# Kernel optimization log

Measured on AMD Instinct MI355X. Metric: run time of the kernel, lower is better.

## Reference

```python
import jax, jax.numpy as jnp
import numpy as np

DIM = 1024
B, S = 4, 4096

def setup_inputs() -> dict:
    key = jax.random.key(0)
    ks = jax.random.split(key, 8)
    scale = 1.0 / np.sqrt(DIM)
    x = jax.random.normal(ks[0], (B, S, DIM), dtype=jnp.float32)
    Wk = jax.random.normal(ks[1], (DIM, DIM), dtype=jnp.float32) * scale
    Wv = jax.random.normal(ks[2], (DIM, DIM), dtype=jnp.float32) * scale
    Wr = jax.random.normal(ks[3], (DIM, DIM), dtype=jnp.float32) * scale
    Wo = jax.random.normal(ks[4], (DIM, DIM), dtype=jnp.float32) * scale
    time_decay = jax.random.normal(ks[5], (DIM,), dtype=jnp.float32) * 0.01 - 5.0
    time_first = jax.random.normal(ks[6], (DIM,), dtype=jnp.float32) * 0.01
    return {"x": x, "Wk": Wk, "Wv": Wv, "Wr": Wr, "Wo": Wo,
            "time_decay": time_decay, "time_first": time_first}

def reference(x, Wk, Wv, Wr, Wo, time_decay, time_first):
    # Projections (Linear with weight [out, in]: y = x @ W^T)
    k = jnp.einsum('bsd,ed->bse', x, Wk)
    v = jnp.einsum('bsd,ed->bse', x, Wv)
    r = jax.nn.sigmoid(jnp.einsum('bsd,ed->bse', x, Wr))
    w = -jnp.exp(time_decay)          # (D,)
    decay = jnp.exp(w)                # exp(w), per-channel decay in (0,1)
    eu = jnp.exp(time_first)          # exp(u)
    kv = k * v                        # (B, S, D)

    def step(state, kv_t):
        wkv = state + eu * kv_t       # output numerator this step
        new_state = decay * state + kv_t
        return new_state, wkv

    state0 = jnp.zeros((x.shape[0], x.shape[2]), dtype=x.dtype)
    # scan over time axis: move S to leading dim
    _, wkv_seq = jax.lax.scan(step, state0, jnp.swapaxes(kv, 0, 1))  # (S, B, D)
    out = r * jnp.swapaxes(wkv_seq, 0, 1)  # (B, S, D)
    return jnp.einsum('bsd,ed->bse', out, Wo)
```

## Files before the change

### kernel.cpp

```cpp
#include <hip/hip_runtime.h>
#include <hip/hip_bf16.h>

#define DIMD   1024
#define BATCH  4
#define SEQ    4096
#define NTOK   (BATCH * SEQ)
#define CHUNK  64
#define NCHUNK (SEQ / CHUNK)

#define BM 128
#define BN 128
#define BK 32
#define BNF 64

typedef unsigned short ushort_t;
typedef __attribute__((ext_vector_type(8))) __bf16   bf16x8;
typedef __attribute__((ext_vector_type(4))) float    f32x4;
typedef __attribute__((ext_vector_type(8))) ushort_t u16x8;

__device__ __forceinline__ float b2f(ushort_t u) {
    union { unsigned int i; float f; } x;
    x.i = ((unsigned int)u) << 16;
    return x.f;
}

__device__ __forceinline__ ushort_t f2b(float f) {
    union { float f; unsigned int i; } x;
    x.f = f;
    unsigned int r = x.i + 0x7fffu + ((x.i >> 16) & 1u);
    return (ushort_t)(r >> 16);
}

__global__ __launch_bounds__(256)
void conv_f2b(const float* __restrict__ src, ushort_t* __restrict__ dst, int n8)
{
    const int i = blockIdx.x * 256 + threadIdx.x;
    if (i >= n8) return;
    const float4* s4 = (const float4*)src;
    const float4 a = s4[i * 2];
    const float4 b = s4[i * 2 + 1];
    u16x8 o;
    o[0] = f2b(a.x); o[1] = f2b(a.y); o[2] = f2b(a.z); o[3] = f2b(a.w);
    o[4] = f2b(b.x); o[5] = f2b(b.y); o[6] = f2b(b.z); o[7] = f2b(b.w);
    *(u16x8*)(dst + (size_t)i * 8) = o;
}

__global__ __launch_bounds__(256)
void conv_w(const float* __restrict__ W0, const float* __restrict__ W1,
            const float* __restrict__ W2, const float* __restrict__ W3,
            ushort_t* __restrict__ dst)
{
    const int m = blockIdx.y;
    const float* src = (m == 0) ? W0 : (m == 1) ? W1 : (m == 2) ? W2 : W3;
    const int i = blockIdx.x * 256 + threadIdx.x;
    const float4* s4 = (const float4*)src;
    const float4 a = s4[i * 2];
    const float4 b = s4[i * 2 + 1];
    u16x8 o;
    o[0] = f2b(a.x); o[1] = f2b(a.y); o[2] = f2b(a.z); o[3] = f2b(a.w);
    o[4] = f2b(b.x); o[5] = f2b(b.y); o[6] = f2b(b.z); o[7] = f2b(b.w);
    *(u16x8*)(dst + (size_t)m * DIMD * DIMD + (size_t)i * 8) = o;
}

__global__ __launch_bounds__(256, 2)
void gemm_kvr(const ushort_t* __restrict__ A,
              const ushort_t* __restrict__ Wk,
              const ushort_t* __restrict__ Wv,
              const ushort_t* __restrict__ Wr,
              const float* __restrict__ td,
              ushort_t* __restrict__ Okv,
              ushort_t* __restrict__ Or,
              float* __restrict__ cs)
{
    __shared__ __align__(16) ushort_t As[BM * BK];
    __shared__ __align__(16) ushort_t Bk[BNF * BK];
    __shared__ __align__(16) ushort_t Bv[BNF * BK];
    __shared__ __align__(16) ushort_t Br[BNF * BK];

    const int tid  = threadIdx.x;
    const int lane = tid & 63;
    const int wv   = tid >> 6;
    const int wr   = wv >> 1;
    const int wc   = wv & 1;
    const int lrow = lane & 15;
    const int kq   = lane >> 4;

    const int row0 = blockIdx.x * BM;
    const int e0   = blockIdx.y * BNF;

    f32x4 ak[4][2], av[4][2], ar[4][2];
#pragma unroll
    for (int i = 0; i < 4; i++)
#pragma unroll
        for (int j = 0; j < 2; j++) {
            ak[i][j] = f32x4{0.f, 0.f, 0.f, 0.f};
            av[i][j] = f32x4{0.f, 0.f, 0.f, 0.f};
            ar[i][j] = f32x4{0.f, 0.f, 0.f, 0.f};
        }

    for (int kt = 0; kt < DIMD / BK; ++kt) {
        const int k0 = kt * BK;

        __syncthreads();

#pragma unroll
        for (int it = 0; it < 2; ++it) {
            const int chunk = tid + it * 256;
            const int r = chunk >> 2;
            const int c = (chunk & 3) << 3;
            const ushort_t* ga = A + (size_t)(row0 + r) * DIMD + k0 + c;
            __builtin_amdgcn_global_load_lds(
                (__attribute__((address_space(1))) void*)ga,
                (__attribute__((address_space(3))) void*)((char*)As + chunk * 16),
                16, 0, 0);
        }
        {
            const int r = tid >> 2;
            const int c = (tid & 3) << 3;
            const size_t go = (size_t)(e0 + r) * DIMD + k0 + c;
            __builtin_amdgcn_global_load_lds(
                (__attribute__((address_space(1))) void*)(Wk + go),
                (__attribute__((address_space(3))) void*)((char*)Bk + tid * 16),
                16, 0, 0);
            __builtin_amdgcn_global_load_lds(
                (__attribute__((address_space(1))) void*)(Wv + go),
                (__attribute__((address_space(3))) void*)((char*)Bv + tid * 16),
                16, 0, 0);
            __builtin_amdgcn_global_load_lds(
                (__attribute__((address_space(1))) void*)(Wr + go),
                (__attribute__((address_space(3))) void*)((char*)Br + tid * 16),
                16, 0, 0);
        }

        __syncthreads();

        bf16x8 af[4], bk4[2], bv4[2], br4[2];
#pragma unroll
        for (int i = 0; i < 4; i++)
            af[i] = *(const bf16x8*)(As + (wr * 64 + i * 16 + lrow) * BK + kq * 8);
#pragma unroll
        for (int j = 0; j < 2; j++) {
            const int bo = (wc * 32 + j * 16 + lrow) * BK + kq * 8;
            bk4[j] = *(const bf16x8*)(Bk + bo);
            bv4[j] = *(const bf16x8*)(Bv + bo);
            br4[j] = *(const bf16x8*)(Br + bo);
        }

#pragma unroll
        for (int i = 0; i < 4; i++)
#pragma unroll
            for (int j = 0; j < 2; j++) {
                ak[i][j] = __builtin_amdgcn_mfma_f32_16x16x32_bf16(
                    af[i], bk4[j], ak[i][j], 0, 0, 0);
                av[i][j] = __builtin_amdgcn_mfma_f32_16x16x32_bf16(
                    af[i], bv4[j], av[i][j], 0, 0, 0);
                ar[i][j] = __builtin_amdgcn_mfma_f32_16x16x32_bf16(
                    af[i], br4[j], ar[i][j], 0, 0, 0);
            }
    }

#pragma unroll
    for (int i = 0; i < 4; i++)
#pragma unroll
        for (int j = 0; j < 2; j++)
#pragma unroll
            for (int r = 0; r < 4; r++) {
                const int row = row0 + wr * 64 + i * 16 + kq * 4 + r;
                const int col = e0 + wc * 32 + j * 16 + lrow;
                const size_t o = (size_t)row * DIMD + col;
                Okv[o] = f2b(ak[i][j][r] * av[i][j][r]);
                Or[o]  = f2b(1.f / (1.f + __expf(-ar[i][j][r])));
            }

#pragma unroll
    for (int j = 0; j < 2; j++) {
        const int col = e0 + wc * 32 + j * 16 + lrow;
        const float w = -__expf(td[col]);
        float s = 0.f;
#pragma unroll
        for (int i = 0; i < 4; i++)
#pragma unroll
            for (int r = 0; r < 4; r++) {
                const int rl = i * 16 + kq * 4 + r;
                s += __expf(w * (float)(63 - rl)) * ak[i][j][r] * av[i][j][r];
            }
        s += __shfl_xor(s, 16);
        s += __shfl_xor(s, 32);
        if (kq == 0) {
            const int gchunk = (row0 >> 6) + wr;
            cs[(size_t)gchunk * DIMD + col] = s;
        }
    }
}

__global__ __launch_bounds__(256, 2)
void gemm_bt(const ushort_t* __restrict__ A,
             const ushort_t* __restrict__ W,
             float* __restrict__ Of)
{
    __shared__ __align__(16) ushort_t As[BM * BK];
    __shared__ __align__(16) ushort_t Bs[BN * BK];

    const int tid  = threadIdx.x;
    const int lane = tid & 63;
    const int wv   = tid >> 6;
    const int wr   = wv >> 1;
    const int wc   = wv & 1;
    const int lrow = lane & 15;
    const int kq   = lane >> 4;

    const int row0 = blockIdx.x * BM;
    const int e0   = blockIdx.y * BN;

    f32x4 acc[4][4];
#pragma unroll
    for (int i = 0; i < 4; i++)
#pragma unroll
        for (int j = 0; j < 4; j++)
            acc[i][j] = f32x4{0.f, 0.f, 0.f, 0.f};

    for (int kt = 0; kt < DIMD / BK; ++kt) {
        const int k0 = kt * BK;

        __syncthreads();

#pragma unroll
        for (int it = 0; it < 2; ++it) {
            const int chunk = tid + it * 256;
            const int r = chunk >> 2;
            const int c = (chunk & 3) << 3;
            const ushort_t* ga = A + (size_t)(row0 + r) * DIMD + k0 + c;
            const ushort_t* gb = W + (size_t)(e0 + r) * DIMD + k0 + c;
            __builtin_amdgcn_global_load_lds(
                (__attribute__((address_space(1))) void*)ga,
                (__attribute__((address_space(3))) void*)((char*)As + chunk * 16),
                16, 0, 0);
            __builtin_amdgcn_global_load_lds(
                (__attribute__((address_space(1))) void*)gb,
                (__attribute__((address_space(3))) void*)((char*)Bs + chunk * 16),
                16, 0, 0);
        }

        __syncthreads();

        bf16x8 af[4], bfr[4];
#pragma unroll
        for (int i = 0; i < 4; i++)
            af[i] = *(const bf16x8*)(As + (wr * 64 + i * 16 + lrow) * BK + kq * 8);
#pragma unroll
        for (int j = 0; j < 4; j++)
            bfr[j] = *(const bf16x8*)(Bs + (wc * 64 + j * 16 + lrow) * BK + kq * 8);

#pragma unroll
        for (int i = 0; i < 4; i++)
#pragma unroll
            for (int j = 0; j < 4; j++)
                acc[i][j] = __builtin_amdgcn_mfma_f32_16x16x32_bf16(
                    af[i], bfr[j], acc[i][j], 0, 0, 0);
    }

#pragma unroll
    for (int i = 0; i < 4; i++)
#pragma unroll
        for (int j = 0; j < 4; j++)
#pragma unroll
            for (int r = 0; r < 4; r++) {
                const int row = row0 + wr * 64 + i * 16 + kq * 4 + r;
                const int col = e0 + wc * 64 + j * 16 + lrow;
                Of[(size_t)row * DIMD + col] = acc[i][j][r];
            }
}

__global__ __launch_bounds__(256)
void chunk_scan(float* __restrict__ cs, const float* __restrict__ td)
{
    const int idx = blockIdx.x * 256 + threadIdx.x;
    const int d = idx & (DIMD - 1);
    const int b = idx >> 10;

    const float w      = -__expf(td[d]);
    const float decayL = __expf(w * (float)CHUNK);

    float v[NCHUNK];
    const size_t base = ((size_t)b * NCHUNK) * DIMD + d;
#pragma unroll
    for (int c = 0; c < NCHUNK; c++)
        v[c] = cs[base + (size_t)c * DIMD];

    float st = 0.f;
#pragma unroll
    for (int c = 0; c < NCHUNK; c++) {
        const float sc = v[c];
        v[c] = st;
        st = decayL * st + sc;
    }

#pragma unroll
    for (int c = 0; c < NCHUNK; c++)
        cs[base + (size_t)c * DIMD] = v[c];
}

__global__ __launch_bounds__(256)
void emit(const ushort_t* __restrict__ kvb, const ushort_t* __restrict__ rb,
          const float* __restrict__ td, const float* __restrict__ tf,
          const float* __restrict__ cs, ushort_t* __restrict__ op)
{
    const int t  = blockIdx.x * 256 + threadIdx.x;
    const int d0 = (t & (DIMD / 8 - 1)) * 8;
    const int bc = t >> 7;
    const int c  = bc & (NCHUNK - 1);
    const int b  = bc >> 6;

    float decay[8], eu[8], st[8];
#pragma unroll
    for (int j = 0; j < 8; j++) {
        decay[j] = __expf(-__expf(td[d0 + j]));
        eu[j]    = __expf(tf[d0 + j]);
    }
    const float* csp = cs + ((size_t)bc * DIMD + d0);
    const float4 s0 = *(const float4*)csp;
    const float4 s1 = *(const float4*)(csp + 4);
    st[0] = s0.x; st[1] = s0.y; st[2] = s0.z; st[3] = s0.w;
    st[4] = s1.x; st[5] = s1.y; st[6] = s1.z; st[7] = s1.w;

    size_t off = ((size_t)b * SEQ + (size_t)c * CHUNK) * DIMD + d0;
#pragma unroll 8
    for (int i = 0; i < CHUNK; i++) {
        const u16x8 kv8 = *(const u16x8*)(kvb + off);
        const u16x8 r8  = *(const u16x8*)(rb + off);
        u16x8 o8;
#pragma unroll
        for (int j = 0; j < 8; j++) {
            const float kv = b2f(kv8[j]);
            o8[j] = f2b(b2f(r8[j]) * (st[j] + eu[j] * kv));
            st[j] = decay[j] * st[j] + kv;
        }
        *(u16x8*)(op + off) = o8;
        off += DIMD;
    }
}

extern "C" void kernel_launch(void* const* d_in, const int* in_sizes, int n_in,
                              void* d_out, int out_size, void* d_ws, size_t ws_size,
                              hipStream_t stream)
{
    const float* x  = (const float*)d_in[0];
    const float* Wk = (const float*)d_in[1];
    const float* Wv = (const float*)d_in[2];
    const float* Wr = (const float*)d_in[3];
    const float* Wo = (const float*)d_in[4];
    const float* td = (const float*)d_in[5];
    const float* tf = (const float*)d_in[6];

    ushort_t* xb  = (ushort_t*)d_ws;
    ushort_t* Wb  = xb + (size_t)NTOK * DIMD;
    ushort_t* Wkb = Wb;
    ushort_t* Wvb = Wb + (size_t)DIMD * DIMD;
    ushort_t* Wrb = Wb + 2 * (size_t)DIMD * DIMD;
    ushort_t* Wob = Wb + 3 * (size_t)DIMD * DIMD;
    float*    cs  = (float*)(Wb + 4 * (size_t)DIMD * DIMD);
    ushort_t* pbuf = xb;

    ushort_t* kvb = (ushort_t*)d_out;
    ushort_t* rb  = kvb + (size_t)NTOK * DIMD;
    float*    out = (float*)d_out;

    conv_f2b<<<NTOK * DIMD / 8 / 256, 256, 0, stream>>>(x, xb, NTOK * DIMD / 8);
    conv_w<<<dim3(DIMD * DIMD / 8 / 256, 4), 256, 0, stream>>>(Wk, Wv, Wr, Wo, Wb);

    gemm_kvr<<<dim3(NTOK / BM, DIMD / BNF), 256, 0, stream>>>(
        xb, Wkb, Wvb, Wrb, td, kvb, rb, cs);

    chunk_scan<<<BATCH * DIMD / 256, 256, 0, stream>>>(cs, td);

    emit<<<BATCH * NCHUNK * (DIMD / 8) / 256, 256, 0, stream>>>(
        kvb, rb, td, tf, cs, pbuf);

    gemm_bt<<<dim3(NTOK / BM, DIMD / BN), 256, 0, stream>>>(pbuf, Wob, out);
}
```

Measured before the change: 314.5 us.

## Double-buffer GEMMs with XOR-swizzled LDS, 512-thread blocks and larger tiles

Both projection GEMMs now use 512-thread blocks with a BK=64, double-buffered global-to-LDS pipeline. Loads for the next k-tile are issued between MFMA phases, with explicit vmcnt/lgkmcnt waits, barriers and setprio. LDS layout is XOR-swizzled to avoid bank conflicts. The output GEMM grows from 128x128 to 256x256 tiles, and the scan/emit kernels switch to 64-thread blocks for more blocks. The change targets global-load latency and barrier stalls in the GEMMs. It risks higher register and LDS pressure (the output GEMM holds 32 accumulators plus 128 KB of LDS) and correctness fragility from the hand-tuned waitcnt counts.

```diff
diff --git a/kernel.cpp b/kernel.cpp
--- a/kernel.cpp
+++ b/kernel.cpp
@@ -8,10 +8,8 @@
 #define CHUNK  64
 #define NCHUNK (SEQ / CHUNK)
 
-#define BM 128
-#define BN 128
-#define BK 32
-#define BNF 64
+#define KBK    64
+#define NKT    (DIMD / KBK)
 
 typedef unsigned short ushort_t;
 typedef __attribute__((ext_vector_type(8))) __bf16   bf16x8;
@@ -30,6 +28,10 @@
     unsigned int r = x.i + 0x7fffu + ((x.i >> 16) & 1u);
     return (ushort_t)(r >> 16);
 }
+
+#define GLL(gsrc, ldst) __builtin_amdgcn_global_load_lds( \
+    (__attribute__((address_space(1))) void*)(gsrc), \
+    (__attribute__((address_space(3))) void*)(ldst), 16, 0, 0)
 
 __global__ __launch_bounds__(256)
 void conv_f2b(const float* __restrict__ src, ushort_t* __restrict__ dst, int n8)
@@ -62,7 +64,7 @@
     *(u16x8*)(dst + (size_t)m * DIMD * DIMD + (size_t)i * 8) = o;
 }
 
-__global__ __launch_bounds__(256, 2)
+__global__ __launch_bounds__(512, 2)
 void gemm_kvr(const ushort_t* __restrict__ A,
               const ushort_t* __restrict__ Wk,
               const ushort_t* __restrict__ Wv,
@@ -72,10 +74,10 @@
               ushort_t* __restrict__ Or,
               float* __restrict__ cs)
 {
-    __shared__ __align__(16) ushort_t As[BM * BK];
-    __shared__ __align__(16) ushort_t Bk[BNF * BK];
-    __shared__ __align__(16) ushort_t Bv[BNF * BK];
-    __shared__ __align__(16) ushort_t Br[BNF * BK];
+    __shared__ __align__(16) ushort_t As[2][256 * KBK];
+    __shared__ __align__(16) ushort_t Bk[2][64 * KBK];
+    __shared__ __align__(16) ushort_t Bv[2][64 * KBK];
+    __shared__ __align__(16) ushort_t Br[2][64 * KBK];
 
     const int tid  = threadIdx.x;
     const int lane = tid & 63;
@@ -84,79 +86,138 @@
     const int wc   = wv & 1;
     const int lrow = lane & 15;
     const int kq   = lane >> 4;
-
-    const int row0 = blockIdx.x * BM;
-    const int e0   = blockIdx.y * BNF;
-
-    f32x4 ak[4][2], av[4][2], ar[4][2];
+    const int s8   = lrow & 7;
+    const int sw0  = (kq ^ s8) * 8;
+    const int sw1  = ((kq + 4) ^ s8) * 8;
+
+    const int row0 = blockIdx.x * 256;
+    const int e0   = blockIdx.y * 64;
+
+    const int r_  = tid >> 3;
+    const int q_  = ((tid & 7) ^ (r_ & 7)) * 8;
+    const size_t aoffs = (size_t)(row0 + r_) * DIMD + q_;
+    const size_t boffs = (size_t)(e0 + r_) * DIMD + q_;
+
+#define KVR_STAGE_A(dst, k0) do { \
+    _Pragma("unroll") \
+    for (int it_ = 0; it_ < 4; ++it_) \
+        GLL(A + aoffs + (size_t)it_ * 64 * DIMD + (k0), \
+            (char*)(dst) + (tid + it_ * 512) * 16); \
+} while (0)
+
+#define KVR_STAGE_B(dk, dv, dr, k0) do { \
+    GLL(Wk + boffs + (k0), (char*)(dk) + tid * 16); \
+    GLL(Wv + boffs + (k0), (char*)(dv) + tid * 16); \
+    GLL(Wr + boffs + (k0), (char*)(dr) + tid * 16); \
+} while (0)
+
+    f32x4 ak[4][2], av[4][2], aR[4][2];
 #pragma unroll
     for (int i = 0; i < 4; i++)
 #pragma unroll
         for (int j = 0; j < 2; j++) {
             ak[i][j] = f32x4{0.f, 0.f, 0.f, 0.f};
             av[i][j] = f32x4{0.f, 0.f, 0.f, 0.f};
-            ar[i][j] = f32x4{0.f, 0.f, 0.f, 0.f};
+            aR[i][j] = f32x4{0.f, 0.f, 0.f, 0.f};
         }
 
-    for (int kt = 0; kt < DIMD / BK; ++kt) {
-        const int k0 = kt * BK;
-
-        __syncthreads();
-
-#pragma unroll
-        for (int it = 0; it < 2; ++it) {
-            const int chunk = tid + it * 256;
-            const int r = chunk >> 2;
-            const int c = (chunk & 3) << 3;
-            const ushort_t* ga = A + (size_t)(row0 + r) * DIMD + k0 + c;
-            __builtin_amdgcn_global_load_lds(
-                (__attribute__((address_space(1))) void*)ga,
-                (__attribute__((address_space(3))) void*)((char*)As + chunk * 16),
-                16, 0, 0);
+    KVR_STAGE_A(&As[0][0], 0);
+    KVR_STAGE_B(&Bk[0][0], &Bv[0][0], &Br[0][0], 0);
+    asm volatile("" ::: "memory");
+    KVR_STAGE_A(&As[1][0], KBK);
+    asm volatile("s_waitcnt vmcnt(4)" ::: "memory");
+    __builtin_amdgcn_s_barrier();
+
+    auto tile = [&](int kt, ushort_t* Asb, ushort_t* Bkb, ushort_t* Bvb,
+                    ushort_t* Brb, ushort_t* Bkn, ushort_t* Bvn, ushort_t* Brn) {
+        bf16x8 af0[4], af1[4], b0[2], b1[2], c0[2], c1[2], d0[2], d1[2];
+
+#pragma unroll
+        for (int i = 0; i < 4; i++)
+            af0[i] = *(const bf16x8*)(Asb + (wr * 64 + i * 16 + lrow) * KBK + sw0);
+#pragma unroll
+        for (int j = 0; j < 2; j++) {
+            const int bo = (wc * 32 + j * 16 + lrow) * KBK + sw0;
+            b0[j] = *(const bf16x8*)(Bkb + bo);
+            c0[j] = *(const bf16x8*)(Bvb + bo);
         }
-        {
-            const int r = tid >> 2;
-            const int c = (tid & 3) << 3;
-            const size_t go = (size_t)(e0 + r) * DIMD + k0 + c;
-            __builtin_amdgcn_global_load_lds(
-                (__attribute__((address_space(1))) void*)(Wk + go),
-                (__attribute__((address_space(3))) void*)((char*)Bk + tid * 16),
-                16, 0, 0);
-            __builtin_amdgcn_global_load_lds(
-                (__attribute__((address_space(1))) void*)(Wv + go),
-                (__attribute__((address_space(3))) void*)((char*)Bv + tid * 16),
-                16, 0, 0);
-            __builtin_amdgcn_global_load_lds(
-                (__attribute__((address_space(1))) void*)(Wr + go),
-                (__attribute__((address_space(3))) void*)((char*)Br + tid * 16),
-                16, 0, 0);
+        if (kt + 1 < NKT) KVR_STAGE_B(Bkn, Bvn, Brn, (kt + 1) * KBK);
+        __builtin_amdgcn_s_barrier();
+        asm volatile("s_waitcnt lgkmcnt(0)" ::: "memory");
+        __builtin_amdgcn_sched_barrier(0);
+        __builtin_amdgcn_s_setprio(1);
+#pragma unroll
+        for (int i = 0; i < 4; i++)
+#pragma unroll
+            for (int j = 0; j < 2; j++) {
+                ak[i][j] = __builtin_amdgcn_mfma_f32_16x16x32_bf16(af0[i], b0[j], ak[i][j], 0, 0, 0);
+                av[i][j] = __builtin_amdgcn_mfma_f32_16x16x32_bf16(af0[i], c0[j], av[i][j], 0, 0, 0);
+            }
+        __builtin_amdgcn_s_setprio(0);
+        __builtin_amdgcn_s_barrier();
+
+#pragma unroll
+        for (int j = 0; j < 2; j++)
+            d0[j] = *(const bf16x8*)(Brb + (wc * 32 + j * 16 + lrow) * KBK + sw0);
+#pragma unroll
+        for (int i = 0; i < 4; i++)
+            af1[i] = *(const bf16x8*)(Asb + (wr * 64 + i * 16 + lrow) * KBK + sw1);
+        __builtin_amdgcn_s_barrier();
+        asm volatile("s_waitcnt lgkmcnt(0)" ::: "memory");
+        __builtin_amdgcn_sched_barrier(0);
+        __builtin_amdgcn_s_setprio(1);
+#pragma unroll
+        for (int i = 0; i < 4; i++)
+#pragma unroll
+            for (int j = 0; j < 2; j++)
+                aR[i][j] = __builtin_amdgcn_mfma_f32_16x16x32_bf16(af0[i], d0[j], aR[i][j], 0, 0, 0);
+        __builtin_amdgcn_s_setprio(0);
+        __builtin_amdgcn_s_barrier();
+
+#pragma unroll
+        for (int j = 0; j < 2; j++) {
+            const int bo = (wc * 32 + j * 16 + lrow) * KBK + sw1;
+            b1[j] = *(const bf16x8*)(Bkb + bo);
+            c1[j] = *(const bf16x8*)(Bvb + bo);
         }
-
-        __syncthreads();
-
-        bf16x8 af[4], bk4[2], bv4[2], br4[2];
-#pragma unroll
-        for (int i = 0; i < 4; i++)
-            af[i] = *(const bf16x8*)(As + (wr * 64 + i * 16 + lrow) * BK + kq * 8);
-#pragma unroll
-        for (int j = 0; j < 2; j++) {
-            const int bo = (wc * 32 + j * 16 + lrow) * BK + kq * 8;
-            bk4[j] = *(const bf16x8*)(Bk + bo);
-            bv4[j] = *(const bf16x8*)(Bv + bo);
-            br4[j] = *(const bf16x8*)(Br + bo);
-        }
-
+        if (kt + 2 < NKT) KVR_STAGE_A(Asb, (kt + 2) * KBK);
+        __builtin_amdgcn_s_barrier();
+        asm volatile("s_waitcnt lgkmcnt(0)" ::: "memory");
+        __builtin_amdgcn_sched_barrier(0);
+        __builtin_amdgcn_s_setprio(1);
 #pragma unroll
         for (int i = 0; i < 4; i++)
 #pragma unroll
             for (int j = 0; j < 2; j++) {
-                ak[i][j] = __builtin_amdgcn_mfma_f32_16x16x32_bf16(
-                    af[i], bk4[j], ak[i][j], 0, 0, 0);
-                av[i][j] = __builtin_amdgcn_mfma_f32_16x16x32_bf16(
-                    af[i], bv4[j], av[i][j], 0, 0, 0);
-                ar[i][j] = __builtin_amdgcn_mfma_f32_16x16x32_bf16(
-                    af[i], br4[j], ar[i][j], 0, 0, 0);
+                ak[i][j] = __builtin_amdgcn_mfma_f32_16x16x32_bf16(af1[i], b1[j], ak[i][j], 0, 0, 0);
+                av[i][j] = __builtin_amdgcn_mfma_f32_16x16x32_bf16(af1[i], c1[j], av[i][j], 0, 0, 0);
             }
+        __builtin_amdgcn_s_setprio(0);
+        __builtin_amdgcn_s_barrier();
+
+#pragma unroll
+        for (int j = 0; j < 2; j++)
+            d1[j] = *(const bf16x8*)(Brb + (wc * 32 + j * 16 + lrow) * KBK + sw1);
+        __builtin_amdgcn_s_barrier();
+        asm volatile("s_waitcnt lgkmcnt(0)" ::: "memory");
+        __builtin_amdgcn_sched_barrier(0);
+        __builtin_amdgcn_s_setprio(1);
+#pragma unroll
+        for (int i = 0; i < 4; i++)
+#pragma unroll
+            for (int j = 0; j < 2; j++)
+                aR[i][j] = __builtin_amdgcn_mfma_f32_16x16x32_bf16(af1[i], d1[j], aR[i][j], 0, 0, 0);
+        __builtin_amdgcn_s_setprio(0);
+        if (kt < NKT - 2)       asm volatile("s_waitcnt vmcnt(4)" ::: "memory");
+        else if (kt == NKT - 2) asm volatile("s_waitcnt vmcnt(0)" ::: "memory");
+        __builtin_amdgcn_s_barrier();
+    };
+
+    for (int m = 0; m < NKT / 2; ++m) {
+        tile(2 * m,     &As[0][0], &Bk[0][0], &Bv[0][0], &Br[0][0],
+                        &Bk[1][0], &Bv[1][0], &Br[1][0]);
+        tile(2 * m + 1, &As[1][0], &Bk[1][0], &Bv[1][0], &Br[1][0],
+                        &Bk[0][0], &Bv[0][0], &Br[0][0]);
     }
 
 #pragma unroll
@@ -169,7 +230,7 @@
                 const int col = e0 + wc * 32 + j * 16 + lrow;
                 const size_t o = (size_t)row * DIMD + col;
                 Okv[o] = f2b(ak[i][j][r] * av[i][j][r]);
-                Or[o]  = f2b(1.f / (1.f + __expf(-ar[i][j][r])));
+                Or[o]  = f2b(1.f / (1.f + __expf(-aR[i][j][r])));
             }
 
 #pragma unroll
@@ -191,90 +252,162 @@
             cs[(size_t)gchunk * DIMD + col] = s;
         }
     }
-}
-
-__global__ __launch_bounds__(256, 2)
+#undef KVR_STAGE_A
+#undef KVR_STAGE_B
+}
+
+__global__ __launch_bounds__(512, 2)
 void gemm_bt(const ushort_t* __restrict__ A,
              const ushort_t* __restrict__ W,
              float* __restrict__ Of)
 {
-    __shared__ __align__(16) ushort_t As[BM * BK];
-    __shared__ __align__(16) ushort_t Bs[BN * BK];
+    __shared__ __align__(16) ushort_t As[2][256 * KBK];
+    __shared__ __align__(16) ushort_t Bs[2][256 * KBK];
 
     const int tid  = threadIdx.x;
     const int lane = tid & 63;
     const int wv   = tid >> 6;
-    const int wr   = wv >> 1;
-    const int wc   = wv & 1;
+    const int wr   = wv >> 2;
+    const int wc   = wv & 3;
     const int lrow = lane & 15;
     const int kq   = lane >> 4;
-
-    const int row0 = blockIdx.x * BM;
-    const int e0   = blockIdx.y * BN;
-
-    f32x4 acc[4][4];
-#pragma unroll
-    for (int i = 0; i < 4; i++)
+    const int s8   = lrow & 7;
+    const int sw0  = (kq ^ s8) * 8;
+    const int sw1  = ((kq + 4) ^ s8) * 8;
+
+    const int row0 = blockIdx.x * 256;
+    const int e0   = blockIdx.y * 256;
+
+    const int r_  = tid >> 3;
+    const int q_  = ((tid & 7) ^ (r_ & 7)) * 8;
+    const size_t aoffs = (size_t)(row0 + r_) * DIMD + q_;
+    const size_t boffs = (size_t)(e0 + r_) * DIMD + q_;
+
+#define BT_STAGE_A(dst, k0) do { \
+    _Pragma("unroll") \
+    for (int it_ = 0; it_ < 4; ++it_) \
+        GLL(A + aoffs + (size_t)it_ * 64 * DIMD + (k0), \
+            (char*)(dst) + (tid + it_ * 512) * 16); \
+} while (0)
+
+#define BT_STAGE_B(dst, k0) do { \
+    _Pragma("unroll") \
+    for (int it_ = 0; it_ < 4; ++it_) \
+        GLL(W + boffs + (size_t)it_ * 64 * DIMD + (k0), \
+            (char*)(dst) + (tid + it_ * 512) * 16); \
+} while (0)
+
+    f32x4 acc[8][4];
+#pragma unroll
+    for (int i = 0; i < 8; i++)
 #pragma unroll
         for (int j = 0; j < 4; j++)
             acc[i][j] = f32x4{0.f, 0.f, 0.f, 0.f};
 
-    for (int kt = 0; kt < DIMD / BK; ++kt) {
-        const int k0 = kt * BK;
-
-        __syncthreads();
-
-#pragma unroll
-        for (int it = 0; it < 2; ++it) {
-            const int chunk = tid + it * 256;
-            const int r = chunk >> 2;
-            const int c = (chunk & 3) << 3;
-            const ushort_t* ga = A + (size_t)(row0 + r) * DIMD + k0 + c;
-            const ushort_t* gb = W + (size_t)(e0 + r) * DIMD + k0 + c;
-            __builtin_amdgcn_global_load_lds(
-                (__attribute__((address_space(1))) void*)ga,
-                (__attribute__((address_space(3))) void*)((char*)As + chunk * 16),
-                16, 0, 0);
-            __builtin_amdgcn_global_load_lds(
-                (__attribute__((address_space(1))) void*)gb,
-                (__attribute__((address_space(3))) void*)((char*)Bs + chunk * 16),
-                16, 0, 0);
-        }
-
-        __syncthreads();
-
-        bf16x8 af[4], bfr[4];
-#pragma unroll
-        for (int i = 0; i < 4; i++)
-            af[i] = *(const bf16x8*)(As + (wr * 64 + i * 16 + lrow) * BK + kq * 8);
+    BT_STAGE_A(&As[0][0], 0);
+    BT_STAGE_B(&Bs[0][0], 0);
+    asm volatile("" ::: "memory");
+    BT_STAGE_A(&As[1][0], KBK);
+    asm volatile("s_waitcnt vmcnt(4)" ::: "memory");
+    __builtin_amdgcn_s_barrier();
+
+    auto tile = [&](int kt, ushort_t* Asb, ushort_t* Bsb, ushort_t* Bsn) {
+        bf16x8 af0[8], af1[8], bf0[4], bf1[4];
+
+#pragma unroll
+        for (int i = 0; i < 8; i++)
+            af0[i] = *(const bf16x8*)(Asb + (wr * 128 + i * 16 + lrow) * KBK + sw0);
+#pragma unroll
+        for (int j = 0; j < 2; j++)
+            bf0[j] = *(const bf16x8*)(Bsb + (wc * 64 + j * 16 + lrow) * KBK + sw0);
+        if (kt + 1 < NKT) BT_STAGE_B(Bsn, (kt + 1) * KBK);
+        __builtin_amdgcn_s_barrier();
+        asm volatile("s_waitcnt lgkmcnt(0)" ::: "memory");
+        __builtin_amdgcn_sched_barrier(0);
+        __builtin_amdgcn_s_setprio(1);
+#pragma unroll
+        for (int i = 0; i < 8; i++)
+#pragma unroll
+            for (int j = 0; j < 2; j++)
+                acc[i][j] = __builtin_amdgcn_mfma_f32_16x16x32_bf16(af0[i], bf0[j], acc[i][j], 0, 0, 0);
+        __builtin_amdgcn_s_setprio(0);
+        __builtin_amdgcn_s_barrier();
+
+#pragma unroll
+        for (int j = 2; j < 4; j++)
+            bf0[j] = *(const bf16x8*)(Bsb + (wc * 64 + j * 16 + lrow) * KBK + sw0);
+        __builtin_amdgcn_s_barrier();
+        asm volatile("s_waitcnt lgkmcnt(0)" ::: "memory");
+        __builtin_amdgcn_sched_barrier(0);
+        __builtin_amdgcn_s_setprio(1);
+#pragma unroll
+        for (int i = 0; i < 8; i++)
+#pragma unroll
+            for (int j = 2; j < 4; j++)
+                acc[i][j] = __builtin_amdgcn_mfma_f32_16x16x32_bf16(af0[i], bf0[j], acc[i][j], 0, 0, 0);
+        __builtin_amdgcn_s_setprio(0);
+        __builtin_amdgcn_s_barrier();
+
+#pragma unroll
+        for (int i = 0; i < 8; i++)
+            af1[i] = *(const bf16x8*)(Asb + (wr * 128 + i * 16 + lrow) * KBK + sw1);
+#pragma unroll
+        for (int j = 0; j < 2; j++)
+            bf1[j] = *(const bf16x8*)(Bsb + (wc * 64 + j * 16 + lrow) * KBK + sw1);
+        __builtin_amdgcn_s_barrier();
+        asm volatile("s_waitcnt lgkmcnt(0)" ::: "memory");
+        __builtin_amdgcn_sched_barrier(0);
+        __builtin_amdgcn_s_setprio(1);
+#pragma unroll
+        for (int i = 0; i < 8; i++)
+#pragma unroll
+            for (int j = 0; j < 2; j++)
+                acc[i][j] = __builtin_amdgcn_mfma_f32_16x16x32_bf16(af1[i], bf1[j], acc[i][j], 0, 0, 0);
+        __builtin_amdgcn_s_setprio(0);
+        __builtin_amdgcn_s_barrier();
+
+#pragma unroll
+        for (int j = 2; j < 4; j++)
+            bf1[j] = *(const bf16x8*)(Bsb + (wc * 64 + j * 16 + lrow) * KBK + sw1);
+        if (kt + 2 < NKT) BT_STAGE_A(Asb, (kt + 2) * KBK);
+        __builtin_amdgcn_s_barrier();
+        asm volatile("s_waitcnt lgkmcnt(0)" ::: "memory");
+        __builtin_amdgcn_sched_barrier(0);
+        __builtin_amdgcn_s_setprio(1);
+#pragma unroll
+        for (int i = 0; i < 8; i++)
+#pragma unroll
+            for (int j = 2; j < 4; j++)
+                acc[i][j] = __builtin_amdgcn_mfma_f32_16x16x32_bf16(af1[i], bf1[j], acc[i][j], 0, 0, 0);
+        __builtin_amdgcn_s_setprio(0);
+        if (kt < NKT - 2)       asm volatile("s_waitcnt vmcnt(4)" ::: "memory");
+        else if (kt == NKT - 2) asm volatile("s_waitcnt vmcnt(0)" ::: "memory");
+        __builtin_amdgcn_s_barrier();
+    };
+
+    for (int m = 0; m < NKT / 2; ++m) {
+        tile(2 * m,     &As[0][0], &Bs[0][0], &Bs[1][0]);
+        tile(2 * m + 1, &As[1][0], &Bs[1][0], &Bs[0][0]);
+    }
+
+#pragma unroll
+    for (int i = 0; i < 8; i++)
 #pragma unroll
         for (int j = 0; j < 4; j++)
-            bfr[j] = *(const bf16x8*)(Bs + (wc * 64 + j * 16 + lrow) * BK + kq * 8);
-
-#pragma unroll
-        for (int i = 0; i < 4; i++)
-#pragma unroll
-            for (int j = 0; j < 4; j++)
-                acc[i][j] = __builtin_amdgcn_mfma_f32_16x16x32_bf16(
-                    af[i], bfr[j], acc[i][j], 0, 0, 0);
-    }
-
-#pragma unroll
-    for (int i = 0; i < 4; i++)
-#pragma unroll
-        for (int j = 0; j < 4; j++)
 #pragma unroll
             for (int r = 0; r < 4; r++) {
-                const int row = row0 + wr * 64 + i * 16 + kq * 4 + r;
+                const int row = row0 + wr * 128 + i * 16 + kq * 4 + r;
                 const int col = e0 + wc * 64 + j * 16 + lrow;
                 Of[(size_t)row * DIMD + col] = acc[i][j][r];
             }
-}
-
-__global__ __launch_bounds__(256)
+#undef BT_STAGE_A
+#undef BT_STAGE_B
+}
+
+__global__ __launch_bounds__(64)
 void chunk_scan(float* __restrict__ cs, const float* __restrict__ td)
 {
-    const int idx = blockIdx.x * 256 + threadIdx.x;
+    const int idx = blockIdx.x * 64 + threadIdx.x;
     const int d = idx & (DIMD - 1);
     const int b = idx >> 10;
 
@@ -300,12 +433,12 @@
         cs[base + (size_t)c * DIMD] = v[c];
 }
 
-__global__ __launch_bounds__(256)
+__global__ __launch_bounds__(64)
 void emit(const ushort_t* __restrict__ kvb, const ushort_t* __restrict__ rb,
           const float* __restrict__ td, const float* __restrict__ tf,
           const float* __restrict__ cs, ushort_t* __restrict__ op)
 {
-    const int t  = blockIdx.x * 256 + threadIdx.x;
+    const int t  = blockIdx.x * 64 + threadIdx.x;
     const int d0 = (t & (DIMD / 8 - 1)) * 8;
     const int bc = t >> 7;
     const int c  = bc & (NCHUNK - 1);
@@ -368,13 +501,13 @@
     conv_f2b<<<NTOK * DIMD / 8 / 256, 256, 0, stream>>>(x, xb, NTOK * DIMD / 8);
     conv_w<<<dim3(DIMD * DIMD / 8 / 256, 4), 256, 0, stream>>>(Wk, Wv, Wr, Wo, Wb);
 
-    gemm_kvr<<<dim3(NTOK / BM, DIMD / BNF), 256, 0, stream>>>(
+    gemm_kvr<<<dim3(NTOK / 256, DIMD / 64), 512, 0, stream>>>(
         xb, Wkb, Wvb, Wrb, td, kvb, rb, cs);
 
-    chunk_scan<<<BATCH * DIMD / 256, 256, 0, stream>>>(cs, td);
-
-    emit<<<BATCH * NCHUNK * (DIMD / 8) / 256, 256, 0, stream>>>(
+    chunk_scan<<<BATCH * DIMD / 64, 64, 0, stream>>>(cs, td);
+
+    emit<<<BATCH * NCHUNK * (DIMD / 8) / 64, 64, 0, stream>>>(
         kvb, rb, td, tf, cs, pbuf);
 
-    gemm_bt<<<dim3(NTOK / BM, DIMD / BN), 256, 0, stream>>>(pbuf, Wob, out);
-}
+    gemm_bt<<<dim3(NTOK / 256, DIMD / 256), 512, 0, stream>>>(pbuf, Wob, out);
+}
```

Measured after the change: 309.4 us. About the same (-1.6%).
